# Performance work log

Hardware: AMD Instinct MI355X
Metric: run time of the kernel (lower is better)

The kernel has to match this reference:

```python
import jax, jax.numpy as jnp
import numpy as np

B, T, M, S, D, H, DH, P = 4, 1024, 1024, 1024, 1024, 16, 64, 4096


def layernorm(x, g, b, eps=1e-5):
    mu = x.mean(-1, keepdims=True)
    var = ((x - mu) ** 2).mean(-1, keepdims=True)
    return (x - mu) * jax.lax.rsqrt(var + eps) * g + b


def rel_shift(x):
    # Transformer-XL relative shift on [B,H,q,k] BD scores
    b, h, q, k = x.shape
    x = jnp.pad(x, ((0, 0), (0, 0), (0, 0), (1, 0)))
    return x.reshape(b, h, k + 1, q)[:, :, 1:, :].reshape(b, h, q, k)


def rel_attention(x, kv, mem, mask, pos_emb, r_w_bias, r_r_bias,
                  Wq, Wk, Wv, Wr, Wo, g, bln):
    # x: [B,Tq,D] queries; kv: [B,Skv,D]; mem: optional [B,M,D]
    cat = kv if mem is None else jnp.concatenate([mem, kv], axis=1)
    Bb, Tq, _ = x.shape
    K = cat.shape[1]
    q = (x @ Wq).reshape(Bb, Tq, H, DH)
    k = (cat @ Wk).reshape(Bb, K, H, DH)
    v = (cat @ Wv).reshape(Bb, K, H, DH)
    r = (pos_emb[-K:] @ Wr).reshape(K, H, DH)  # rel-pos keys, most-recent K positions
    AC = jnp.einsum('bthd,bkhd->bhtk', q + r_w_bias, k)
    BD = rel_shift(jnp.einsum('bthd,khd->bhtk', q + r_r_bias, r))
    scores = (AC + BD) * (1.0 / np.sqrt(DH))
    scores = jnp.where(mask[:, None, :, :], jnp.asarray(-1e30, scores.dtype), scores)
    prob = jax.nn.softmax(scores, axis=-1)
    o = jnp.einsum('bhtk,bkhd->bthd', prob, v).reshape(Bb, Tq, H * DH) @ Wo
    return layernorm(x + o, g, bln), cat, prob  # post-LN residual; cat is new memory


def residual_ff(x, W1, b1, W2, b2, g, bln):
    h = jax.nn.relu(x @ W1 + b1) @ W2 + b2
    return layernorm(x + h, g, bln)


def setup_inputs() -> dict:
    key = jax.random.key(0)
    ks = jax.random.split(key, 24)
    w = lambda i, shape: jax.random.normal(ks[i], shape, jnp.float32) * 0.02
    causal = jnp.triu(jnp.ones((T, M + T), bool), k=M + 1)  # True = masked
    return {
        'src': jax.random.normal(ks[0], (B, S, D), jnp.float32),
        'tgt': jax.random.normal(ks[1], (B, T, D), jnp.float32),
        'tgt_mem': jax.random.normal(ks[2], (B, M, D), jnp.float32),
        'pos_emb': w(3, (M + T, D)),
        'r_w_bias': w(4, (H, DH)),
        'r_r_bias': w(5, (H, DH)),
        'Wq1': w(6, (D, H * DH)), 'Wk1': w(7, (D, H * DH)), 'Wv1': w(8, (D, H * DH)),
        'Wr1': w(9, (D, H * DH)), 'Wo1': w(10, (H * DH, D)),
        'ln1_g': jnp.ones((D,), jnp.float32), 'ln1_b': jnp.zeros((D,), jnp.float32),
        'Wq2': w(11, (D, H * DH)), 'Wk2': w(12, (D, H * DH)), 'Wv2': w(13, (D, H * DH)),
        'Wr2': w(14, (D, H * DH)), 'Wo2': w(15, (H * DH, D)),
        'ln2_g': jnp.ones((D,), jnp.float32), 'ln2_b': jnp.zeros((D,), jnp.float32),
        'Wf1': w(16, (D, P)), 'bf1': jnp.zeros((P,), jnp.float32),
        'Wf2': w(17, (P, D)), 'bf2': jnp.zeros((D,), jnp.float32),
        'ln3_g': jnp.ones((D,), jnp.float32), 'ln3_b': jnp.zeros((D,), jnp.float32),
        'tgt_mask': jnp.broadcast_to(causal, (B, T, M + T)),
        'tgt_to_src_mask': jnp.zeros((B, T, S), bool),
    }


def reference(src, tgt, tgt_mem, pos_emb, r_w_bias, r_r_bias,
              Wq1, Wk1, Wv1, Wr1, Wo1, ln1_g, ln1_b,
              Wq2, Wk2, Wv2, Wr2, Wo2, ln2_g, ln2_b,
              Wf1, bf1, Wf2, bf2, ln3_g, ln3_b,
              tgt_mask, tgt_to_src_mask):
    out, new_mem, self_att_prob = rel_attention(
        tgt, tgt, tgt_mem, tgt_mask, pos_emb, r_w_bias, r_r_bias,
        Wq1, Wk1, Wv1, Wr1, Wo1, ln1_g, ln1_b)
    out, _, inter_att_prob = rel_attention(
        out, src, None, tgt_to_src_mask, pos_emb, r_w_bias, r_r_bias,
        Wq2, Wk2, Wv2, Wr2, Wo2, ln2_g, ln2_b)
    out = residual_ff(out, Wf1, bf1, Wf2, bf2, ln3_g, ln3_b)
    return (out, new_mem, self_att_prob, inter_att_prob)
```

## Files before the change

kernel.cpp:

```cpp
#include <hip/hip_runtime.h>

typedef unsigned short u16;
typedef __attribute__((ext_vector_type(8))) short short8;
typedef __attribute__((ext_vector_type(4))) float f4;
typedef __attribute__((ext_vector_type(4))) unsigned short u16x4;

__device__ __forceinline__ float b2f(u16 u) {
    unsigned int x = ((unsigned int)u) << 16;
    return __builtin_bit_cast(float, x);
}
__device__ __forceinline__ u16 f2b(float f) {
    unsigned int u = __builtin_bit_cast(unsigned int, f);
    u += 0x7FFFu + ((u >> 16) & 1u);
    return (u16)(u >> 16);
}

__device__ __forceinline__ void gl16(const void* g, void* l) {
    __builtin_amdgcn_global_load_lds(
        (const __attribute__((address_space(1))) void*)g,
        (__attribute__((address_space(3))) void*)l, 16, 0, 0);
}

template<int FM, int FN, int CBF, int EPI>
__global__ __launch_bounds__(256, 3)
void gemm_bt(const u16* __restrict__ Ap, const u16* __restrict__ Bp,
             void* __restrict__ Cp, const float* __restrict__ bias,
             int M, int N, int K, int lda, int ldb, int ldc,
             long long sAh, long long sAb, long long sBh, long long sBb,
             long long sCh, long long sCb, int batchH)
{
    constexpr int BM = FM * 32;
    constexpr int BN = FN * 32;
    __shared__ __align__(16) u16 As[2][BM * 32];
    __shared__ __align__(16) u16 Bs[2][BN * 32];

    const int tid  = threadIdx.x;
    const int z    = blockIdx.z;
    const int bb   = z / batchH;
    const int hh   = z - bb * batchH;
    const int m0   = blockIdx.y * BM;
    const int n0   = blockIdx.x * BN;
    const int w    = tid >> 6;
    const int lane = tid & 63;
    const int wr   = w >> 1;
    const int wc   = w & 1;
    const int lrow = lane & 15;
    const int lk   = (lane >> 4) << 3;
    const int lrow4 = lane >> 2;
    const int lch   = lane & 3;

    const u16* Ag = Ap + sAb * bb + sAh * hh;
    const u16* Bg = Bp + sBb * bb + sBh * hh;

    f4 acc[FM][FN] = {};

    auto stage = [&](int buf, int kt) {
        const int kb = kt << 5;
        #pragma unroll
        for (int i = 0; i < BM / 64; ++i) {
            const int row0 = (w + i * 4) << 4;
            gl16(Ag + (long long)(m0 + row0 + lrow4) * lda + kb + (lch << 3),
                 &As[buf][row0 * 32]);
        }
        #pragma unroll
        for (int i = 0; i < BN / 64; ++i) {
            const int row0 = (w + i * 4) << 4;
            gl16(Bg + (long long)(n0 + row0 + lrow4) * ldb + kb + (lch << 3),
                 &Bs[buf][row0 * 32]);
        }
    };

    const int nKt = K >> 5;
    stage(0, 0);
    __syncthreads();
    int cur = 0;
    for (int kt = 0; kt < nKt; ++kt) {
        if (kt + 1 < nKt) stage(cur ^ 1, kt + 1);

        short8 af[FM], bv[FN];
        #pragma unroll
        for (int m = 0; m < FM; ++m)
            af[m] = *(const short8*)(&As[cur][(wr * FM * 16 + m * 16 + lrow) * 32 + lk]);
        #pragma unroll
        for (int n = 0; n < FN; ++n)
            bv[n] = *(const short8*)(&Bs[cur][(wc * FN * 16 + n * 16 + lrow) * 32 + lk]);
        #pragma unroll
        for (int m = 0; m < FM; ++m)
            #pragma unroll
            for (int n = 0; n < FN; ++n)
                acc[m][n] = __builtin_amdgcn_mfma_f32_16x16x32_bf16(af[m], bv[n], acc[m][n], 0, 0, 0);

        __syncthreads();
        cur ^= 1;
    }

    const int crow0 = m0 + wr * FM * 16 + ((lane >> 4) << 2);
    const int ccol0 = n0 + wc * FN * 16 + lrow;
    if (CBF == 0) {
        float* Cg = (float*)Cp + sCb * bb + sCh * hh;
        #pragma unroll
        for (int m = 0; m < FM; ++m) {
            #pragma unroll
            for (int n = 0; n < FN; ++n) {
                const int col = ccol0 + n * 16;
                float bvv = (EPI >= 1) ? bias[col] : 0.f;
                #pragma unroll
                for (int r = 0; r < 4; ++r) {
                    float vv = acc[m][n][r] + bvv;
                    if (EPI == 2) vv = fmaxf(vv, 0.f);
                    Cg[(long long)(crow0 + m * 16 + r) * ldc + col] = vv;
                }
            }
        }
    } else {
        u16* Cg = (u16*)Cp + sCb * bb + sCh * hh;
        #pragma unroll
        for (int m = 0; m < FM; ++m) {
            #pragma unroll
            for (int n = 0; n < FN; ++n) {
                const int col = ccol0 + n * 16;
                float bvv = (EPI >= 1) ? bias[col] : 0.f;
                #pragma unroll
                for (int r = 0; r < 4; ++r) {
                    float vv = acc[m][n][r] + bvv;
                    if (EPI == 2) vv = fmaxf(vv, 0.f);
                    Cg[(long long)(crow0 + m * 16 + r) * ldc + col] = f2b(vv);
                }
            }
        }
    }
}

template<int KK, int MODE>
__global__ __launch_bounds__(512)
void fattn(const u16* __restrict__ qsrc, long long qld, long long qsb,
           const float* __restrict__ rwb, const float* __restrict__ rrb,
           const u16* __restrict__ kb, const u16* __restrict__ rr,
           const u16* __restrict__ vt,
           float* __restrict__ probs, u16* __restrict__ ob, int kld)
{
    constexpr int LE = KK + 8;
    constexpr int NT = KK / 16;
    __shared__ __align__(16) u16 e[16 * LE];
    __shared__ __align__(16) u16 qws[16 * 72];
    __shared__ __align__(16) u16 qrs[17 * 72];
    __shared__ float psum[8][16];

    const int tid = threadIdx.x;
    const int bh  = blockIdx.y;
    const int b   = bh >> 4, h = bh & 15;
    const int t0  = blockIdx.x << 4;

    if (tid < 264) {
        int row, ch; const float* bias; u16* dst; bool act = true;
        if (tid < 128)      { row = tid >> 3;        ch = tid & 7; bias = rwb; dst = &qws[row * 72 + ch * 8]; }
        else if (tid < 256) { row = (tid - 128) >> 3; ch = tid & 7; bias = rrb; dst = &qrs[row * 72 + ch * 8]; }
        else if (MODE == 1) { row = 16;              ch = tid - 256; bias = rrb; dst = &qrs[16 * 72 + ch * 8]; }
        else act = false;
        if (act) {
            int trow = t0 + row; if (trow > 1023) trow = 1023;
            short8 qv = *(const short8*)(qsrc + b * qsb + (long long)trow * qld + h * 64 + ch * 8);
            const float* bp = bias + h * 64 + ch * 8;
            f4 b0 = *(const f4*)bp, b1 = *(const f4*)(bp + 4);
            short8 o;
            o[0] = (short)f2b((b2f((u16)qv[0]) + b0.x) * 0.125f);
            o[1] = (short)f2b((b2f((u16)qv[1]) + b0.y) * 0.125f);
            o[2] = (short)f2b((b2f((u16)qv[2]) + b0.z) * 0.125f);
            o[3] = (short)f2b((b2f((u16)qv[3]) + b0.w) * 0.125f);
            o[4] = (short)f2b((b2f((u16)qv[4]) + b1.x) * 0.125f);
            o[5] = (short)f2b((b2f((u16)qv[5]) + b1.y) * 0.125f);
            o[6] = (short)f2b((b2f((u16)qv[6]) + b1.z) * 0.125f);
            o[7] = (short)f2b((b2f((u16)qv[7]) + b1.w) * 0.125f);
            *(short8*)dst = o;
        }
    }
    __syncthreads();

    const int w = tid >> 6, lane = tid & 63;
    const int lc = lane & 15, g = lane >> 4, lk = g << 3;
    const int t = t0 + lc;

    const short8 bq0 = *(const short8*)&qws[lc * 72 + lk];
    const short8 bq1 = *(const short8*)&qws[lc * 72 + 32 + lk];
    const short8 br0 = *(const short8*)&qrs[lc * 72 + lk];
    const short8 br1 = *(const short8*)&qrs[lc * 72 + 32 + lk];
    short8 bs0 = {}, bs1 = {};
    if (MODE == 1) {
        bs0 = *(const short8*)&qrs[(lc + 1) * 72 + lk];
        bs1 = *(const short8*)&qrs[(lc + 1) * 72 + 32 + lk];
    }

    #pragma unroll 2
    for (int ut = w; ut < NT; ut += 8) {
        const int u0 = ut << 4;
        const bool need1 = (u0 + t0 + 30 >= 1023);
        const bool need2 = (MODE == 1) && (u0 + t0 <= 1021);
        if (!need1 && !need2) continue;
        const u16* rg = rr + (long long)(u0 + lc) * 2048 + h * 64;
        const short8 a0 = *(const short8*)(rg + lk);
        const short8 a1 = *(const short8*)(rg + 32 + lk);
        if (need1) {
            f4 acc = {};
            acc = __builtin_amdgcn_mfma_f32_16x16x32_bf16(a0, br0, acc, 0, 0, 0);
            acc = __builtin_amdgcn_mfma_f32_16x16x32_bf16(a1, br1, acc, 0, 0, 0);
            #pragma unroll
            for (int i = 0; i < 4; ++i) {
                const int j = u0 + 4 * g + i + t - 1023;
                if (j >= 0) e[lc * LE + j] = f2b(acc[i]);
            }
        }
        if (MODE == 1 && need2) {
            f4 acc = {};
            acc = __builtin_amdgcn_mfma_f32_16x16x32_bf16(a0, bs0, acc, 0, 0, 0);
            acc = __builtin_amdgcn_mfma_f32_16x16x32_bf16(a1, bs1, acc, 0, 0, 0);
            #pragma unroll
            for (int i = 0; i < 4; ++i) {
                const int j = u0 + 4 * g + i + t + 2;
                if (j < KK) e[lc * LE + j] = f2b(acc[i]);
            }
        }
    }
    __syncthreads();

    float sum = 0.f;
    const int limit = t + 1024;
    const int jvt = (MODE == 0) ? ((t0 + 1039) >> 4) : (NT - 1);
    #pragma unroll 4
    for (int jt = w; jt < NT; jt += 8) {
        const int j0 = jt << 4;
        const int jme = j0 + 4 * g;
        if (MODE == 0 && jt > jvt) {
            u16x4 z = {0, 0, 0, 0};
            *(u16x4*)&e[lc * LE + jme] = z;
            continue;
        }
        const u16* kg = kb + (long long)(b * KK + j0 + lc) * kld + h * 64;
        const short8 a0 = *(const short8*)(kg + lk);
        const short8 a1 = *(const short8*)(kg + 32 + lk);
        f4 acc = {};
        acc = __builtin_amdgcn_mfma_f32_16x16x32_bf16(a0, bq0, acc, 0, 0, 0);
        acc = __builtin_amdgcn_mfma_f32_16x16x32_bf16(a1, bq1, acc, 0, 0, 0);
        u16x4 bd4 = *(const u16x4*)&e[lc * LE + jme];
        u16x4 st;
        #pragma unroll
        for (int i = 0; i < 4; ++i) {
            const int j = jme + i;
            float bd = b2f(bd4[i]);
            if (MODE == 1 && j == t + 1) bd = 0.f;
            float ev = __expf(acc[i] + bd);
            if (MODE == 0 && j > limit) ev = 0.f;
            sum += ev;
            st[i] = f2b(ev);
        }
        *(u16x4*)&e[lc * LE + jme] = st;
    }
    sum += __shfl_xor(sum, 16);
    sum += __shfl_xor(sum, 32);
    if (g == 0) psum[w][lc] = sum;
    __syncthreads();

    if (w >= 4) {
        const int r = (tid >> 4) & 15;
        const int q = tid & 15;
        float s = 0.f;
        #pragma unroll
        for (int w2 = 0; w2 < 8; ++w2) s += psum[w2][r];
        const float inv = 1.f / s;
        float* pr = probs + ((long long)bh * 1024 + t0 + r) * KK;
        #pragma unroll 4
        for (int i2 = 0; i2 < KK / 128; ++i2) {
            const int j0 = q * 8 + i2 * 128;
            u16x4 e0 = *(const u16x4*)&e[r * LE + j0];
            u16x4 e1 = *(const u16x4*)&e[r * LE + j0 + 4];
            f4 p0, p1;
            p0.x = b2f(e0.x) * inv; p0.y = b2f(e0.y) * inv;
            p0.z = b2f(e0.z) * inv; p0.w = b2f(e0.w) * inv;
            p1.x = b2f(e1.x) * inv; p1.y = b2f(e1.y) * inv;
            p1.z = b2f(e1.z) * inv; p1.w = b2f(e1.w) * inv;
            __builtin_nontemporal_store(p0, (f4*)(pr + j0));
            __builtin_nontemporal_store(p1, (f4*)(pr + j0 + 4));
        }
    } else {
        const int db = w << 4;
        const u16* vrow = vt + ((long long)(bh * 64 + db + lc)) * KK + lk;
        int kcend = KK / 32;
        if (MODE == 0) {
            const int ke = (t0 + 1071) >> 5;
            if (ke < kcend) kcend = ke;
        }
        f4 acc = {};
        #pragma unroll 2
        for (int kc = 0; kc < kcend; ++kc) {
            short8 a = *(const short8*)&e[lc * LE + kc * 32 + lk];
            short8 bv = *(const short8*)(vrow + kc * 32);
            acc = __builtin_amdgcn_mfma_f32_16x16x32_bf16(a, bv, acc, 0, 0, 0);
        }
        #pragma unroll
        for (int i = 0; i < 4; ++i) {
            const int trow = g * 4 + i;
            float s = 0.f;
            #pragma unroll
            for (int w2 = 0; w2 < 8; ++w2) s += psum[w2][trow];
            ob[((long long)(b * 1024 + t0 + trow)) * 1024 + h * 64 + db + lc] = f2b(acc[i] / s);
        }
    }
}

__global__ void conv_f2b(const float* __restrict__ in, u16* __restrict__ out, long long n4)
{
    long long i = (long long)blockIdx.x * 256 + threadIdx.x;
    if (i >= n4) return;
    f4 v = *(const f4*)(in + i * 4);
    u16x4 o; o.x = f2b(v.x); o.y = f2b(v.y); o.z = f2b(v.z); o.w = f2b(v.w);
    *(u16x4*)(out + i * 4) = o;
}

__global__ void concat_mem(const float* __restrict__ mem, const float* __restrict__ tgt,
                           float* __restrict__ nm, u16* __restrict__ cat)
{
    long long i = (long long)blockIdx.x * 256 + threadIdx.x;
    long long b = i >> 19;
    int rem = (int)(i & 524287);
    int r = rem >> 8, c4 = rem & 255;
    const float* sp = (r < 1024) ? (mem + ((b << 10) + r) * 1024 + c4 * 4)
                                 : (tgt + ((b << 10) + (r - 1024)) * 1024 + c4 * 4);
    f4 v = *(const f4*)sp;
    __builtin_nontemporal_store(v, (f4*)(nm + i * 4));
    u16x4 o; o.x = f2b(v.x); o.y = f2b(v.y); o.z = f2b(v.z); o.w = f2b(v.w);
    *(u16x4*)(cat + i * 4) = o;
}

struct TWS { const float* s; u16* d; int sld, dld; };
struct TW18 { TWS t[18]; };
__global__ void transpose_w18(TW18 p)
{
    __shared__ float tile[32][33];
    const TWS ts = p.t[blockIdx.z];
    int c0 = blockIdx.x * 32, r0 = blockIdx.y * 32;
    int tx = threadIdx.x, ty = threadIdx.y;
    tile[ty][tx] = ts.s[(long long)(r0 + ty) * ts.sld + c0 + tx];
    __syncthreads();
    ts.d[(long long)(c0 + ty) * ts.dld + r0 + tx] = f2b(tile[tx][ty]);
}

__global__ __launch_bounds__(256) void transpose_v(const u16* __restrict__ v, u16* __restrict__ vt,
                                                   int KK, int ld, int coff)
{
    __shared__ u16 tile[64][68];
    const int z = blockIdx.z, b = z >> 4, h = z & 15;
    const int j0 = blockIdx.x << 6;
    const int rr8 = threadIdx.x >> 3;
    const int c8 = (threadIdx.x & 7) << 3;
    #pragma unroll
    for (int p = 0; p < 2; ++p) {
        const int jr = p * 32 + rr8;
        short8 val = *(const short8*)(v + ((long long)(b * KK + j0 + jr)) * ld + coff + h * 64 + c8);
        #pragma unroll
        for (int k = 0; k < 8; ++k) tile[c8 + k][jr] = (u16)val[k];
    }
    __syncthreads();
    #pragma unroll
    for (int p = 0; p < 2; ++p) {
        const int d = p * 32 + rr8;
        short8 o;
        #pragma unroll
        for (int k = 0; k < 8; ++k) o[k] = (short)tile[d][c8 + k];
        *(short8*)(vt + ((long long)((b * 16 + h) * 64 + d)) * KK + j0 + c8) = o;
    }
}

__global__ __launch_bounds__(256) void ln_res(const float* __restrict__ x,
                                              const float* __restrict__ h1,
                                              const float* __restrict__ h2,
                                              const float* __restrict__ hbias,
                                              const float* __restrict__ g, const float* __restrict__ bl,
                                              float* __restrict__ o32, u16* __restrict__ obf)
{
    const long long row = blockIdx.x;
    const int tid = threadIdx.x;
    const long long base = row * 1024 + tid * 4;
    f4 xa = *(const f4*)(x + base);
    f4 ha = *(const f4*)(h1 + base);
    f4 hb = *(const f4*)(h2 + base);
    f4 hc = {0.f, 0.f, 0.f, 0.f};
    if (hbias) hc = *(const f4*)(hbias + tid * 4);
    float v0 = xa.x + ha.x + hb.x + hc.x, v1 = xa.y + ha.y + hb.y + hc.y;
    float v2 = xa.z + ha.z + hb.z + hc.z, v3 = xa.w + ha.w + hb.w + hc.w;
    float lsum = v0 + v1 + v2 + v3;
    float lsq = v0 * v0 + v1 * v1 + v2 * v2 + v3 * v3;
    #pragma unroll
    for (int o2 = 32; o2; o2 >>= 1) { lsum += __shfl_xor(lsum, o2); lsq += __shfl_xor(lsq, o2); }
    __shared__ float r1[4], r2[4];
    int w = tid >> 6, lane = tid & 63;
    if (lane == 0) { r1[w] = lsum; r2[w] = lsq; }
    __syncthreads();
    lsum = r1[0] + r1[1] + r1[2] + r1[3];
    lsq  = r2[0] + r2[1] + r2[2] + r2[3];
    const float mu = lsum * 0.0009765625f;
    const float var = lsq * 0.0009765625f - mu * mu;
    const float rsd = rsqrtf(var + 1e-5f);
    const int c = tid * 4;
    f4 gv = *(const f4*)(g + c);
    f4 bv = *(const f4*)(bl + c);
    f4 y;
    y.x = (v0 - mu) * rsd * gv.x + bv.x;
    y.y = (v1 - mu) * rsd * gv.y + bv.y;
    y.z = (v2 - mu) * rsd * gv.z + bv.z;
    y.w = (v3 - mu) * rsd * gv.w + bv.w;
    *(f4*)(o32 + base) = y;
    if (obf) {
        u16x4 u; u.x = f2b(y.x); u.y = f2b(y.y); u.z = f2b(y.z); u.w = f2b(y.w);
        *(u16x4*)(obf + base) = u;
    }
}

extern "C" void kernel_launch(void* const* d_in, const int* in_sizes, int n_in,
                              void* d_out, int out_size, void* d_ws, size_t ws_size,
                              hipStream_t stream)
{
    (void)in_sizes; (void)n_in; (void)out_size;
    const float* src  = (const float*)d_in[0];
    const float* tgt  = (const float*)d_in[1];
    const float* mem  = (const float*)d_in[2];
    const float* pos  = (const float*)d_in[3];
    const float* rwb  = (const float*)d_in[4];
    const float* rrb  = (const float*)d_in[5];
    const float* Wq1  = (const float*)d_in[6];
    const float* Wk1  = (const float*)d_in[7];
    const float* Wv1  = (const float*)d_in[8];
    const float* Wr1  = (const float*)d_in[9];
    const float* Wo1  = (const float*)d_in[10];
    const float* ln1g = (const float*)d_in[11];
    const float* ln1b = (const float*)d_in[12];
    const float* Wq2  = (const float*)d_in[13];
    const float* Wk2  = (const float*)d_in[14];
    const float* Wv2  = (const float*)d_in[15];
    const float* Wr2  = (const float*)d_in[16];
    const float* Wo2  = (const float*)d_in[17];
    const float* ln2g = (const float*)d_in[18];
    const float* ln2b = (const float*)d_in[19];
    const float* Wf1  = (const float*)d_in[20];
    const float* bf1  = (const float*)d_in[21];
    const float* Wf2  = (const float*)d_in[22];
    const float* bf2  = (const float*)d_in[23];
    const float* ln3g = (const float*)d_in[24];
    const float* ln3b = (const float*)d_in[25];

    float* outp   = (float*)d_out;
    float* newmem = outp + 4194304;
    float* selfP  = outp + 12582912;
    float* interP = outp + 146800640;

    char* ws = (char*)d_ws;
    size_t off = 0;
    auto alloc = [&](size_t bytes) -> void* {
        void* p = ws + off;
        off = (off + bytes + 255) & ~(size_t)255;
        return p;
    };
    u16*   src_bf  = (u16*)alloc(8u << 20);
    u16*   cat_bf  = (u16*)alloc(16u << 20);
    u16*   pos_bf  = (u16*)alloc(4u << 20);
    u16*   W1t    = (u16*)alloc(6u << 20);
    u16*   Wr12t  = (u16*)alloc(4u << 20);
    u16*   W2t    = (u16*)alloc(4u << 20);
    u16*   Wq2t   = (u16*)alloc(2u << 20);
    u16*   Wo1t   = (u16*)alloc(2u << 20);
    u16*   Wo2t   = (u16*)alloc(2u << 20);
    u16*   Wf1t   = (u16*)alloc(8u << 20);
    u16*   Wf2t   = (u16*)alloc(8u << 20);
    u16*   P1     = (u16*)alloc(48u << 20);
    u16*   P2k    = (u16*)alloc(8u << 20);
    u16*   P2v    = (u16*)alloc(8u << 20);
    u16*   R12    = (u16*)alloc(8u << 20);
    u16*   qb2    = (u16*)alloc(8u << 20);
    u16*   vtb    = (u16*)alloc(16u << 20);
    u16*   ob     = (u16*)alloc(8u << 20);
    float* projb  = (float*)alloc(16u << 20);
    float* projb2 = (float*)alloc(16u << 20);
    float* out1_32 = (float*)alloc(16u << 20);
    u16*   out1_bf = (u16*)alloc(8u << 20);
    float* out2_32 = (float*)alloc(16u << 20);
    u16*   out2_bf = (u16*)alloc(8u << 20);
    u16*   hb     = (u16*)alloc(32u << 20);
    if (off > ws_size) return;
    const long long PJ2 = projb2 - projb;

    dim3 tb(32, 32);

    concat_mem<<<8192, 256, 0, stream>>>(mem, tgt, newmem, cat_bf);
    conv_f2b<<<4096, 256, 0, stream>>>(src, src_bf, 1048576);
    conv_f2b<<<2048, 256, 0, stream>>>(pos, pos_bf, 524288);
    TW18 tw;
    tw.t[0] = {Wq1, W1t, 1024, 1024};
    tw.t[1] = {Wk1, W1t + 1048576, 1024, 1024};
    tw.t[2] = {Wv1, W1t + 2097152, 1024, 1024};
    tw.t[3] = {Wr1, Wr12t, 1024, 1024};
    tw.t[4] = {Wr2, Wr12t + 1048576, 1024, 1024};
    tw.t[5] = {Wk2, W2t, 1024, 1024};
    tw.t[6] = {Wv2, W2t + 1048576, 1024, 1024};
    tw.t[7] = {Wq2, Wq2t, 1024, 1024};
    tw.t[8] = {Wo1, Wo1t, 1024, 1024};
    tw.t[9] = {Wo2, Wo2t, 1024, 1024};
    for (int zz = 0; zz < 4; ++zz) {
        tw.t[10 + zz] = {Wf1 + zz * 1024, Wf1t + (long long)zz * 1048576, 4096, 1024};
        tw.t[14 + zz] = {Wf2 + (long long)zz * 1048576, Wf2t + zz * 1024, 1024, 4096};
    }
    transpose_w18<<<dim3(32, 32, 18), tb, 0, stream>>>(tw);

    gemm_bt<4,4,1,0><<<dim3(24,64,1), 256, 0, stream>>>(cat_bf, W1t, P1, nullptr,
        8192,3072,1024, 1024,1024,3072, 0,0,0,0,0,0, 1);
    gemm_bt<4,4,1,0><<<dim3(16,16,1), 256, 0, stream>>>(pos_bf, Wr12t, R12, nullptr,
        2048,2048,1024, 1024,1024,2048, 0,0,0,0,0,0, 1);
    transpose_v<<<dim3(32,1,64), 256, 0, stream>>>(P1, vtb, 2048, 3072, 2048);
    fattn<2048,0><<<dim3(64,64), 512, 0, stream>>>(P1 + 1024LL * 3072, 3072LL, 2048LL * 3072,
        rwb, rrb, P1 + 1024, R12, vtb, selfP, ob, 3072);
    gemm_bt<4,4,0,0><<<dim3(8,32,2), 256, 0, stream>>>(ob, Wo1t, projb, nullptr,
        4096,1024,512, 1024,1024,1024, 0,512, 0,512, 0,PJ2, 1);
    ln_res<<<4096, 256, 0, stream>>>(tgt, projb, projb2, nullptr, ln1g, ln1b, out1_32, out1_bf);

    {
        const long long dA = (long long)(src_bf - out1_bf);
        const long long dB1 = (long long)(W2t - Wq2t);
        const long long dB2 = (long long)((W2t + 1048576) - Wq2t);
        const long long dC1 = (long long)(P2k - qb2);
        const long long dC2 = (long long)(P2v - qb2);
        gemm_bt<4,4,1,0><<<dim3(8,32,3), 256, 0, stream>>>(out1_bf, Wq2t, qb2, nullptr,
            4096,1024,1024, 1024,1024,1024, dA,dA, dB1,dB2, dC1,dC2, 2);
    }
    transpose_v<<<dim3(16,1,64), 256, 0, stream>>>(P2v, vtb, 1024, 1024, 0);
    fattn<1024,1><<<dim3(64,64), 512, 0, stream>>>(qb2, 1024LL, 1048576LL,
        rwb, rrb, P2k, R12 + 1024LL * 2048 + 1024, vtb, interP, ob, 1024);
    gemm_bt<4,4,0,0><<<dim3(8,32,2), 256, 0, stream>>>(ob, Wo2t, projb, nullptr,
        4096,1024,512, 1024,1024,1024, 0,512, 0,512, 0,PJ2, 1);
    ln_res<<<4096, 256, 0, stream>>>(out1_32, projb, projb2, nullptr, ln2g, ln2b, out2_32, out2_bf);

    gemm_bt<4,4,1,2><<<dim3(32,32,1), 256, 0, stream>>>(out2_bf, Wf1t, hb, bf1,
        4096,4096,1024, 1024,1024,4096, 0,0,0,0,0,0, 1);
    gemm_bt<4,4,0,0><<<dim3(8,32,2), 256, 0, stream>>>(hb, Wf2t, projb, nullptr,
        4096,1024,2048, 4096,4096,1024, 0,2048, 0,2048, 0,PJ2, 1);
    ln_res<<<4096, 256, 0, stream>>>(out2_32, projb, projb2, bf2, ln3g, ln3b, outp, nullptr);
}
```

Measured before the change: 965.1 us.

## Split self-attn QKV projection to skip memory-row queries, batch K loads in fattn

The fused QKV GEMM over all 8192 cat rows is split in two. A K/V GEMM runs over every row and writes to a padded buffer with row stride 2080. A separate Q GEMM runs only over the 4096 target rows, so the memory rows no longer get a wasted query projection. Inside fattn, the R and K tile loads are hoisted into small register batches ahead of the MFMAs so loads overlap compute, and launch bounds now request 4 waves per SIMD. The risks are higher register pressure and an extra kernel launch.

```diff
diff --git a/kernel.cpp b/kernel.cpp
--- a/kernel.cpp
+++ b/kernel.cpp
@@ -132,7 +132,7 @@
 }
 
 template<int KK, int MODE>
-__global__ __launch_bounds__(512)
+__global__ __launch_bounds__(512, 4)
 void fattn(const u16* __restrict__ qsrc, long long qld, long long qsb,
            const float* __restrict__ rwb, const float* __restrict__ rrb,
            const u16* __restrict__ kb, const u16* __restrict__ rr,
@@ -141,6 +141,7 @@
 {
     constexpr int LE = KK + 8;
     constexpr int NT = KK / 16;
+    constexpr int NI = NT / 8;
     __shared__ __align__(16) u16 e[16 * LE];
     __shared__ __align__(16) u16 qws[16 * 72];
     __shared__ __align__(16) u16 qrs[17 * 72];
@@ -190,33 +191,45 @@
         bs1 = *(const short8*)&qrs[(lc + 1) * 72 + 32 + lk];
     }
 
-    #pragma unroll 2
-    for (int ut = w; ut < NT; ut += 8) {
-        const int u0 = ut << 4;
-        const bool need1 = (u0 + t0 + 30 >= 1023);
-        const bool need2 = (MODE == 1) && (u0 + t0 <= 1021);
-        if (!need1 && !need2) continue;
-        const u16* rg = rr + (long long)(u0 + lc) * 2048 + h * 64;
-        const short8 a0 = *(const short8*)(rg + lk);
-        const short8 a1 = *(const short8*)(rg + 32 + lk);
-        if (need1) {
-            f4 acc = {};
-            acc = __builtin_amdgcn_mfma_f32_16x16x32_bf16(a0, br0, acc, 0, 0, 0);
-            acc = __builtin_amdgcn_mfma_f32_16x16x32_bf16(a1, br1, acc, 0, 0, 0);
-            #pragma unroll
-            for (int i = 0; i < 4; ++i) {
-                const int j = u0 + 4 * g + i + t - 1023;
-                if (j >= 0) e[lc * LE + j] = f2b(acc[i]);
-            }
-        }
-        if (MODE == 1 && need2) {
-            f4 acc = {};
-            acc = __builtin_amdgcn_mfma_f32_16x16x32_bf16(a0, bs0, acc, 0, 0, 0);
-            acc = __builtin_amdgcn_mfma_f32_16x16x32_bf16(a1, bs1, acc, 0, 0, 0);
-            #pragma unroll
-            for (int i = 0; i < 4; ++i) {
-                const int j = u0 + 4 * g + i + t + 2;
-                if (j < KK) e[lc * LE + j] = f2b(acc[i]);
+    #pragma unroll
+    for (int Bb = 0; Bb < NI; Bb += 2) {
+        short8 R0[2], R1[2];
+        #pragma unroll
+        for (int u = 0; u < 2; ++u) {
+            const int ut = w + (Bb + u) * 8;
+            const int u0 = ut << 4;
+            const bool nd = (u0 + t0 + 30 >= 1023) || (MODE == 1 && u0 + t0 <= 1021);
+            if (nd) {
+                const u16* rg = rr + (long long)(u0 + lc) * 2048 + h * 64;
+                R0[u] = *(const short8*)(rg + lk);
+                R1[u] = *(const short8*)(rg + 32 + lk);
+            }
+        }
+        #pragma unroll
+        for (int u = 0; u < 2; ++u) {
+            const int ut = w + (Bb + u) * 8;
+            const int u0 = ut << 4;
+            const bool need1 = (u0 + t0 + 30 >= 1023);
+            const bool need2 = (MODE == 1) && (u0 + t0 <= 1021);
+            if (need1) {
+                f4 acc = {};
+                acc = __builtin_amdgcn_mfma_f32_16x16x32_bf16(R0[u], br0, acc, 0, 0, 0);
+                acc = __builtin_amdgcn_mfma_f32_16x16x32_bf16(R1[u], br1, acc, 0, 0, 0);
+                #pragma unroll
+                for (int i = 0; i < 4; ++i) {
+                    const int j = u0 + 4 * g + i + t - 1023;
+                    if (j >= 0) e[lc * LE + j] = f2b(acc[i]);
+                }
+            }
+            if (MODE == 1 && need2) {
+                f4 acc = {};
+                acc = __builtin_amdgcn_mfma_f32_16x16x32_bf16(R0[u], bs0, acc, 0, 0, 0);
+                acc = __builtin_amdgcn_mfma_f32_16x16x32_bf16(R1[u], bs1, acc, 0, 0, 0);
+                #pragma unroll
+                for (int i = 0; i < 4; ++i) {
+                    const int j = u0 + 4 * g + i + t + 2;
+                    if (j < KK) e[lc * LE + j] = f2b(acc[i]);
+                }
             }
         }
     }
@@ -225,34 +238,44 @@
     float sum = 0.f;
     const int limit = t + 1024;
     const int jvt = (MODE == 0) ? ((t0 + 1039) >> 4) : (NT - 1);
-    #pragma unroll 4
-    for (int jt = w; jt < NT; jt += 8) {
-        const int j0 = jt << 4;
-        const int jme = j0 + 4 * g;
-        if (MODE == 0 && jt > jvt) {
-            u16x4 z = {0, 0, 0, 0};
-            *(u16x4*)&e[lc * LE + jme] = z;
-            continue;
-        }
-        const u16* kg = kb + (long long)(b * KK + j0 + lc) * kld + h * 64;
-        const short8 a0 = *(const short8*)(kg + lk);
-        const short8 a1 = *(const short8*)(kg + 32 + lk);
-        f4 acc = {};
-        acc = __builtin_amdgcn_mfma_f32_16x16x32_bf16(a0, bq0, acc, 0, 0, 0);
-        acc = __builtin_amdgcn_mfma_f32_16x16x32_bf16(a1, bq1, acc, 0, 0, 0);
-        u16x4 bd4 = *(const u16x4*)&e[lc * LE + jme];
-        u16x4 st;
-        #pragma unroll
-        for (int i = 0; i < 4; ++i) {
-            const int j = jme + i;
-            float bd = b2f(bd4[i]);
-            if (MODE == 1 && j == t + 1) bd = 0.f;
-            float ev = __expf(acc[i] + bd);
-            if (MODE == 0 && j > limit) ev = 0.f;
-            sum += ev;
-            st[i] = f2b(ev);
-        }
-        *(u16x4*)&e[lc * LE + jme] = st;
+    #pragma unroll
+    for (int Bb = 0; Bb < NI; Bb += 4) {
+        short8 K0[4], K1[4];
+        #pragma unroll
+        for (int u = 0; u < 4; ++u) {
+            const int jt = w + (Bb + u) * 8;
+            if (MODE != 0 || jt <= jvt) {
+                const u16* kg = kb + (long long)(b * KK + (jt << 4) + lc) * kld + h * 64;
+                K0[u] = *(const short8*)(kg + lk);
+                K1[u] = *(const short8*)(kg + 32 + lk);
+            }
+        }
+        #pragma unroll
+        for (int u = 0; u < 4; ++u) {
+            const int jt = w + (Bb + u) * 8;
+            const int jme = (jt << 4) + 4 * g;
+            if (MODE == 0 && jt > jvt) {
+                u16x4 z = {0, 0, 0, 0};
+                *(u16x4*)&e[lc * LE + jme] = z;
+            } else {
+                f4 acc = {};
+                acc = __builtin_amdgcn_mfma_f32_16x16x32_bf16(K0[u], bq0, acc, 0, 0, 0);
+                acc = __builtin_amdgcn_mfma_f32_16x16x32_bf16(K1[u], bq1, acc, 0, 0, 0);
+                u16x4 bd4 = *(const u16x4*)&e[lc * LE + jme];
+                u16x4 st;
+                #pragma unroll
+                for (int i = 0; i < 4; ++i) {
+                    const int j = jme + i;
+                    float bd = b2f(bd4[i]);
+                    if (MODE == 1 && j == t + 1) bd = 0.f;
+                    float ev = __expf(acc[i] + bd);
+                    if (MODE == 0 && j > limit) ev = 0.f;
+                    sum += ev;
+                    st[i] = f2b(ev);
+                }
+                *(u16x4*)&e[lc * LE + jme] = st;
+            }
+        }
     }
     sum += __shfl_xor(sum, 16);
     sum += __shfl_xor(sum, 32);
@@ -469,7 +492,8 @@
     u16*   Wo2t   = (u16*)alloc(2u << 20);
     u16*   Wf1t   = (u16*)alloc(8u << 20);
     u16*   Wf2t   = (u16*)alloc(8u << 20);
-    u16*   P1     = (u16*)alloc(48u << 20);
+    u16*   P1kv   = (u16*)alloc(34u << 20);
+    u16*   qb1    = (u16*)alloc(8u << 20);
     u16*   P2k    = (u16*)alloc(8u << 20);
     u16*   P2v    = (u16*)alloc(8u << 20);
     u16*   R12    = (u16*)alloc(8u << 20);
@@ -508,13 +532,15 @@
     }
     transpose_w18<<<dim3(32, 32, 18), tb, 0, stream>>>(tw);
 
-    gemm_bt<4,4,1,0><<<dim3(24,64,1), 256, 0, stream>>>(cat_bf, W1t, P1, nullptr,
-        8192,3072,1024, 1024,1024,3072, 0,0,0,0,0,0, 1);
+    gemm_bt<4,4,1,0><<<dim3(16,64,1), 256, 0, stream>>>(cat_bf, W1t + 1048576, P1kv, nullptr,
+        8192,2048,1024, 1024,1024,2080, 0,0,0,0,0,0, 1);
+    gemm_bt<4,4,1,0><<<dim3(8,8,4), 256, 0, stream>>>(cat_bf + 1048576, W1t, qb1, nullptr,
+        1024,1024,1024, 1024,1024,1024, 0,2048LL*1024, 0,0, 0,1048576LL, 1);
     gemm_bt<4,4,1,0><<<dim3(16,16,1), 256, 0, stream>>>(pos_bf, Wr12t, R12, nullptr,
         2048,2048,1024, 1024,1024,2048, 0,0,0,0,0,0, 1);
-    transpose_v<<<dim3(32,1,64), 256, 0, stream>>>(P1, vtb, 2048, 3072, 2048);
-    fattn<2048,0><<<dim3(64,64), 512, 0, stream>>>(P1 + 1024LL * 3072, 3072LL, 2048LL * 3072,
-        rwb, rrb, P1 + 1024, R12, vtb, selfP, ob, 3072);
+    transpose_v<<<dim3(32,1,64), 256, 0, stream>>>(P1kv, vtb, 2048, 2080, 1024);
+    fattn<2048,0><<<dim3(64,64), 512, 0, stream>>>(qb1, 1024LL, 1048576LL,
+        rwb, rrb, P1kv, R12, vtb, selfP, ob, 2080);
     gemm_bt<4,4,0,0><<<dim3(8,32,2), 256, 0, stream>>>(ob, Wo1t, projb, nullptr,
         4096,1024,512, 1024,1024,1024, 0,512, 0,512, 0,PJ2, 1);
     ln_res<<<4096, 256, 0, stream>>>(tgt, projb, projb2, nullptr, ln1g, ln1b, out1_32, out1_bf);
```

Result: faster. 928.3 us (-3.8%).
